# Optimization experiments

Hardware: AMD Instinct MI355X
Metric: run time of the kernel (lower is better)

The kernel has to match this reference:

```python
import jax, jax.numpy as jnp
import numpy as np

B, S, D_IN, D_OUT = 4, 4096, 768, 768

def setup_inputs() -> dict:
    key = jax.random.key(0)
    k1, k2, k3, k4 = jax.random.split(key, 4)
    x = jax.random.normal(k1, (B, S, D_IN), dtype=jnp.float32)
    # Stored as [d_in, d_out]; torch Linear computes x @ W.T with W [d_out, d_in],
    # which is equivalent to x @ W_here for a fresh random init.
    Wq = jax.random.normal(k2, (D_IN, D_OUT), dtype=jnp.float32) * (1.0 / np.sqrt(D_IN))
    Wk = jax.random.normal(k3, (D_IN, D_OUT), dtype=jnp.float32) * (1.0 / np.sqrt(D_IN))
    Wv = jax.random.normal(k4, (D_IN, D_OUT), dtype=jnp.float32) * (1.0 / np.sqrt(D_IN))
    return {"x": x, "Wq": Wq, "Wk": Wk, "Wv": Wv}

def reference(x, Wq, Wk, Wv):
    # x: [B, S, d_in]
    q = jnp.einsum('bsi,io->bso', x, Wq)  # [B, S, d_out]
    k = jnp.einsum('bsi,io->bso', x, Wk)
    v = jnp.einsum('bsi,io->bso', x, Wv)
    scale = 1.0 / jnp.sqrt(jnp.asarray(q.shape[-1], dtype=q.dtype))
    scores = jnp.einsum('bqd,bkd->bqk', q, k)  # [B, S, S]
    S_len = scores.shape[-1]
    causal = jnp.tril(jnp.ones((S_len, S_len), dtype=bool))  # True = keep
    scores = jnp.where(causal[None, :, :], scores, -jnp.inf)
    weights = jax.nn.softmax(scores * scale, axis=-1)
    # dropout p=0.0 -> identity
    return jnp.einsum('bqk,bkd->bqd', weights, v)
```

## Files before the change

### kernel.cpp

```cpp
#include <hip/hip_runtime.h>

typedef __attribute__((ext_vector_type(8))) short short8;
typedef __attribute__((ext_vector_type(4))) float f32x4;
typedef unsigned short u16;

#define MFMA_BF16 __builtin_amdgcn_mfma_f32_16x16x32_bf16

__device__ __forceinline__ u16 f2bf(float f) {
    unsigned int u = __builtin_bit_cast(unsigned int, f);
    u = (u + 0x7FFFu + ((u >> 16) & 1u)) >> 16;
    return (u16)u;
}

__device__ __forceinline__ void gl_lds16(const void* g, void* l) {
    __builtin_amdgcn_global_load_lds(
        (const __attribute__((address_space(1))) unsigned int*)g,
        (__attribute__((address_space(3))) unsigned int*)l, 16, 0, 0);
}

constexpr int D = 768;
constexpr int S = 4096;
constexpr float SCALE = 0.03608439182435161f;

__device__ __forceinline__ void tri_decode(int t, int& i, int& j) {
    i = (int)((sqrtf(8.0f * t + 1.0f) - 1.0f) * 0.5f);
    while ((i + 1) * (i + 2) / 2 <= t) ++i;
    while (i * (i + 1) / 2 > t) --i;
    j = t - i * (i + 1) / 2;
}

__global__ __launch_bounds__(256)
void conv_x(const float* __restrict__ x, u16* __restrict__ xb) {
    const size_t i = ((size_t)blockIdx.x * 256 + threadIdx.x) * 4;
    const float4 v = *reinterpret_cast<const float4*>(x + i);
    ushort4 o;
    o.x = f2bf(v.x); o.y = f2bf(v.y); o.z = f2bf(v.z); o.w = f2bf(v.w);
    *reinterpret_cast<ushort4*>(xb + i) = o;
}

__global__ __launch_bounds__(256)
void conv_wt(const float* __restrict__ Wq, const float* __restrict__ Wk,
             const float* __restrict__ Wv, u16* __restrict__ WT) {
    __shared__ float t[64][65];
    const int tid = threadIdx.x;
    const int k0 = blockIdx.x * 64, n0 = blockIdx.y * 64, z = blockIdx.z;
    const float* __restrict__ W = (z == 0) ? Wq : ((z == 1) ? Wk : Wv);
    #pragma unroll
    for (int i = 0; i < 4; ++i) {
        const int e = (i * 256 + tid) * 4;
        const int r = e >> 6, c = e & 63;
        const float4 v = *reinterpret_cast<const float4*>(W + (size_t)(k0 + r) * D + n0 + c);
        t[r][c] = v.x; t[r][c + 1] = v.y; t[r][c + 2] = v.z; t[r][c + 3] = v.w;
    }
    __syncthreads();
    u16* O = WT + (size_t)z * D * D;
    #pragma unroll
    for (int i = 0; i < 4; ++i) {
        const int e = (i * 256 + tid) * 4;
        const int n = e >> 6, kq = e & 63;
        ushort4 o;
        o.x = f2bf(t[kq + 0][n]); o.y = f2bf(t[kq + 1][n]);
        o.z = f2bf(t[kq + 2][n]); o.w = f2bf(t[kq + 3][n]);
        *reinterpret_cast<ushort4*>(O + (size_t)(n0 + n) * D + k0 + kq) = o;
    }
}

__global__ __launch_bounds__(256)
void qkv_gemm(const u16* __restrict__ xb, const u16* __restrict__ WT,
              u16* __restrict__ qo, u16* __restrict__ ko, u16* __restrict__ vt)
{
    __shared__ u16 sA[2][128 * 32];
    __shared__ u16 sB[2][128 * 32];
    const int tid  = threadIdx.x;
    const int lane = tid & 63;
    const int w    = tid >> 6;
    const int wr   = w >> 1, wc = w & 1;
    const int bm   = blockIdx.x * 128;
    const int bn   = blockIdx.y * 128;
    const int z    = blockIdx.z;
    const u16* __restrict__ A = xb;
    const u16* __restrict__ B = WT + (size_t)z * D * D;

    f32x4 acc[4][4] = {};

    auto stage = [&](int buf, int kc) {
        #pragma unroll
        for (int c = 0; c < 2; ++c) {
            const int e   = (c * 256 + tid) * 8;
            const int row = e >> 5, col = e & 31;
            gl_lds16(A + (size_t)(bm + row) * D + kc * 32 + col, &sA[buf][e]);
            gl_lds16(B + (size_t)(bn + row) * D + kc * 32 + col, &sB[buf][e]);
        }
    };

    stage(0, 0);
    __syncthreads();
    int cur = 0;
    for (int kc = 0; kc < 24; ++kc) {
        if (kc < 23) stage(cur ^ 1, kc + 1);
        short8 af[4], bf4[4];
        #pragma unroll
        for (int fr = 0; fr < 4; ++fr)
            af[fr] = *reinterpret_cast<const short8*>(&sA[cur][(wr * 64 + fr * 16 + (lane & 15)) * 32 + (lane >> 4) * 8]);
        #pragma unroll
        for (int fc = 0; fc < 4; ++fc)
            bf4[fc] = *reinterpret_cast<const short8*>(&sB[cur][(wc * 64 + fc * 16 + (lane & 15)) * 32 + (lane >> 4) * 8]);
        #pragma unroll
        for (int fr = 0; fr < 4; ++fr)
            #pragma unroll
            for (int fc = 0; fc < 4; ++fc)
                acc[fr][fc] = MFMA_BF16(af[fr], bf4[fc], acc[fr][fc], 0, 0, 0);
        __syncthreads();
        cur ^= 1;
    }

    #pragma unroll
    for (int fr = 0; fr < 4; ++fr) {
        #pragma unroll
        for (int fc = 0; fc < 4; ++fc) {
            #pragma unroll
            for (int r = 0; r < 4; ++r) {
                const int m = bm + wr * 64 + fr * 16 + (lane >> 4) * 4 + r;
                const int n = bn + wc * 64 + fc * 16 + (lane & 15);
                const u16 hv = f2bf(acc[fr][fc][r]);
                if (z == 0)      qo[(size_t)m * D + n] = hv;
                else if (z == 1) ko[(size_t)m * D + n] = hv;
                else {
                    const int bb = m >> 12;
                    const int s  = m & (S - 1);
                    vt[((size_t)bb * D + n) * S + s] = hv;
                }
            }
        }
    }
}

__global__ __launch_bounds__(256)
void qkt_gemm(const u16* __restrict__ Qg, const u16* __restrict__ Kg,
              u16* __restrict__ Pp, float* __restrict__ Lp)
{
    __shared__ u16 sA[2][128 * 32];
    __shared__ u16 sB[2][128 * 32];
    const int tid  = threadIdx.x;
    const int lane = tid & 63;
    const int w    = tid >> 6;
    const int wr   = w >> 1, wc = w & 1;
    int ti, tj;
    tri_decode(blockIdx.x, ti, tj);
    const int b = blockIdx.y;
    const u16* __restrict__ A = Qg + ((size_t)b * S + ti * 128) * D;
    const u16* __restrict__ B = Kg + ((size_t)b * S + tj * 128) * D;

    f32x4 acc[4][4] = {};

    auto stage = [&](int buf, int kc) {
        #pragma unroll
        for (int c = 0; c < 2; ++c) {
            const int e   = (c * 256 + tid) * 8;
            const int row = e >> 5, col = e & 31;
            gl_lds16(A + (size_t)row * D + kc * 32 + col, &sA[buf][e]);
            gl_lds16(B + (size_t)row * D + kc * 32 + col, &sB[buf][e]);
        }
    };

    stage(0, 0);
    __syncthreads();
    int cur = 0;
    for (int kc = 0; kc < 24; ++kc) {
        if (kc < 23) stage(cur ^ 1, kc + 1);
        short8 af[4], bf4[4];
        #pragma unroll
        for (int fr = 0; fr < 4; ++fr)
            af[fr] = *reinterpret_cast<const short8*>(&sA[cur][(wr * 64 + fr * 16 + (lane & 15)) * 32 + (lane >> 4) * 8]);
        #pragma unroll
        for (int fc = 0; fc < 4; ++fc)
            bf4[fc] = *reinterpret_cast<const short8*>(&sB[cur][(wc * 64 + fc * 16 + (lane & 15)) * 32 + (lane >> 4) * 8]);
        #pragma unroll
        for (int fr = 0; fr < 4; ++fr)
            #pragma unroll
            for (int fc = 0; fc < 4; ++fc)
                acc[fr][fc] = MFMA_BF16(af[fr], bf4[fc], acc[fr][fc], 0, 0, 0);
        __syncthreads();
        cur ^= 1;
    }

    const bool diag = (ti == tj);
    u16* outT = Pp + ((size_t)b * 528 + blockIdx.x) * 16384;
    #pragma unroll
    for (int fr = 0; fr < 4; ++fr) {
        #pragma unroll
        for (int r = 0; r < 4; ++r) {
            const int m = wr * 64 + fr * 16 + (lane >> 4) * 4 + r;
            float rs = 0.0f;
            #pragma unroll
            for (int fc = 0; fc < 4; ++fc) {
                const int n = wc * 64 + fc * 16 + (lane & 15);
                float p = __expf(acc[fr][fc][r] * SCALE - 10.0f);
                if (diag && n > m) p = 0.0f;
                rs += p;
                outT[m * 128 + n] = f2bf(p);
            }
            rs += __shfl_xor(rs, 1);
            rs += __shfl_xor(rs, 2);
            rs += __shfl_xor(rs, 4);
            rs += __shfl_xor(rs, 8);
            if ((lane & 15) == 0)
                Lp[(((size_t)b * 32 + tj) * 2 + wc) * 4096 + ti * 128 + m] = rs;
        }
    }
}

__global__ __launch_bounds__(256)
void reduce_l(const float* __restrict__ Lp, float* __restrict__ Li)
{
    const int row = blockIdx.x * 256 + threadIdx.x;
    const int b = row >> 12, r = row & 4095, imax = r >> 7;
    float l = 0.0f;
    for (int j = 0; j <= imax; ++j) {
        l += Lp[(((size_t)b * 32 + j) * 2 + 0) * 4096 + r];
        l += Lp[(((size_t)b * 32 + j) * 2 + 1) * 4096 + r];
    }
    Li[row] = 1.0f / l;
}

__global__ __launch_bounds__(512)
void pv_gemm(const u16* __restrict__ Pp, const u16* __restrict__ Vt,
             const float* __restrict__ Li, float* __restrict__ out)
{
    __shared__ u16 sV[2][192 * 64];
    __shared__ u16 sP[2][128 * 64];
    const int tid  = threadIdx.x;
    const int lane = tid & 63;
    const int w    = tid >> 6;
    const int wq   = w >> 2;
    const int wd   = w & 3;
    const int bid  = blockIdx.x;
    const int i    = 31 - (bid >> 4);
    const int b    = (bid >> 2) & 3;
    const int dq   = bid & 3;
    const int q0   = i * 128, d0 = dq * 192;
    const int nkt  = 2 * i + 2;
    const u16* __restrict__ Pt  = Pp + ((size_t)b * 528 + (size_t)i * (i + 1) / 2) * 16384;
    const u16* __restrict__ vtb = Vt + ((size_t)b * D + d0) * S;

    f32x4 acc[4][3] = {};

    auto stage_v = [&](int buf, int kt) {
        #pragma unroll
        for (int n = 0; n < 3; ++n) {
            const int ch  = n * 512 + tid;
            const int row = ch >> 3;
            const int csw = (ch & 7) ^ (row & 7);
            gl_lds16(vtb + (size_t)row * S + kt * 64 + csw * 8, &sV[buf][ch * 8]);
        }
    };
    auto stage_p = [&](int buf, int kt) {
        const u16* base = Pt + (size_t)(kt >> 1) * 16384 + (kt & 1) * 64;
        #pragma unroll
        for (int n = 0; n < 2; ++n) {
            const int ch  = n * 512 + tid;
            const int row = ch >> 3;
            const int csw = (ch & 7) ^ (row & 7);
            gl_lds16(base + row * 128 + csw * 8, &sP[buf][ch * 8]);
        }
    };

    stage_v(0, 0); stage_p(0, 0);
    __syncthreads();
    int cur = 0;
    for (int kt = 0; kt < nkt; ++kt) {
        if (kt + 1 < nkt) { stage_v(cur ^ 1, kt + 1); stage_p(cur ^ 1, kt + 1); }
        #pragma unroll
        for (int ks = 0; ks < 2; ++ks) {
            short8 a[4];
            #pragma unroll
            for (int fr = 0; fr < 4; ++fr) {
                const int row = wq * 64 + fr * 16 + (lane & 15);
                const int cch = (ks * 4 + (lane >> 4)) ^ (row & 7);
                a[fr] = *reinterpret_cast<const short8*>(&sP[cur][row * 64 + cch * 8]);
            }
            #pragma unroll
            for (int fc = 0; fc < 3; ++fc) {
                const int dr  = wd * 48 + fc * 16 + (lane & 15);
                const int vch = (ks * 4 + (lane >> 4)) ^ (dr & 7);
                const short8 bv = *reinterpret_cast<const short8*>(&sV[cur][dr * 64 + vch * 8]);
                #pragma unroll
                for (int fr = 0; fr < 4; ++fr)
                    acc[fr][fc] = MFMA_BF16(a[fr], bv, acc[fr][fc], 0, 0, 0);
            }
        }
        __syncthreads();
        cur ^= 1;
    }

    #pragma unroll
    for (int fr = 0; fr < 4; ++fr)
        #pragma unroll
        for (int rr = 0; rr < 4; ++rr) {
            const int row = q0 + wq * 64 + fr * 16 + (lane >> 4) * 4 + rr;
            const float linv = Li[b * 4096 + row];
            #pragma unroll
            for (int fc = 0; fc < 3; ++fc) {
                const int col = d0 + wd * 48 + fc * 16 + (lane & 15);
                out[((size_t)b * S + row) * D + col] = acc[fr][fc][rr] * linv;
            }
        }
}

extern "C" void kernel_launch(void* const* d_in, const int* in_sizes, int n_in,
                              void* d_out, int out_size, void* d_ws, size_t ws_size,
                              hipStream_t stream) {
    const float* x  = (const float*)d_in[0];
    const float* Wq = (const float*)d_in[1];
    const float* Wk = (const float*)d_in[2];
    const float* Wv = (const float*)d_in[3];
    float* out = (float*)d_out;

    const size_t SD = (size_t)16384 * 768;
    u16* q  = (u16*)d_ws;
    u16* k  = q  + SD;
    u16* vt = k  + SD;
    u16* xb = vt + SD;
    u16* WT = xb + SD;
    u16* Pp = WT + (size_t)3 * 768 * 768;
    float* Lp = (float*)(Pp + (size_t)4 * 528 * 16384);
    float* Li = Lp + (size_t)4 * 32 * 2 * 4096;
    (void)in_sizes; (void)n_in; (void)out_size; (void)ws_size;

    conv_x  <<<12288, 256, 0, stream>>>(x, xb);
    conv_wt <<<dim3(12, 12, 3), 256, 0, stream>>>(Wq, Wk, Wv, WT);
    qkv_gemm<<<dim3(128, 6, 3), 256, 0, stream>>>(xb, WT, q, k, vt);
    qkt_gemm<<<dim3(528, 4), 256, 0, stream>>>(q, k, Pp, Lp);
    reduce_l<<<64, 256, 0, stream>>>(Lp, Li);
    pv_gemm <<<512, 512, 0, stream>>>(Pp, vt, Li, out);
}
```

Baseline: 308.5 us.

## Enlarge QKV and QK^T GEMM tiles with swizzled LDS and deeper pipelining

The QKV projection and the causal QK^T score kernels move to 512-thread blocks with larger tiles (256x192 and 256x256) and K-chunks of 64. Shared memory uses an XOR-swizzled layout, the global-to-LDS loads are explicitly pipelined with vmcnt waits, raw barriers and setprio around the MFMA groups. The V transpose is no longer done by scattered stores in the GEMM epilogue. It becomes a separate LDS-based transpose kernel that uses the P buffer as scratch. The aim is more data reuse per load and less overhead from barriers and uncoalesced stores. The cost is an extra launch, more registers per thread, and extra work on the diagonal tiles that straddle the causal mask.

```diff
diff --git a/kernel.cpp b/kernel.cpp
--- a/kernel.cpp
+++ b/kernel.cpp
@@ -5,6 +5,9 @@
 typedef unsigned short u16;
 
 #define MFMA_BF16 __builtin_amdgcn_mfma_f32_16x16x32_bf16
+#define S_BARRIER()  asm volatile("s_barrier" ::: "memory")
+#define WAIT_LGKM0() asm volatile("s_waitcnt lgkmcnt(0)" ::: "memory")
+#define WAIT_VM(n)   asm volatile("s_waitcnt vmcnt(" #n ")" ::: "memory")
 
 __device__ __forceinline__ u16 f2bf(float f) {
     unsigned int u = __builtin_bit_cast(unsigned int, f);
@@ -27,6 +30,21 @@
     while ((i + 1) * (i + 2) / 2 <= t) ++i;
     while (i * (i + 1) / 2 > t) --i;
     j = t - i * (i + 1) / 2;
+}
+
+template<int NCH>
+__device__ __forceinline__ void stage64(const u16* __restrict__ g, u16* lds, int kcol, int tid) {
+    #pragma unroll
+    for (int i = 0; i < NCH; ++i) {
+        const int ch = i * 512 + tid;
+        const int row = ch >> 3, c = ch & 7;
+        const int cs = c ^ (row & 7);
+        gl_lds16(g + (size_t)row * 768 + kcol + cs * 8, lds + ch * 8);
+    }
+}
+__device__ __forceinline__ short8 ldsfrag(const u16* p, int row, int ks, int lane) {
+    const int cs = (ks * 4 + (lane >> 4)) ^ (row & 7);
+    return *reinterpret_cast<const short8*>(p + row * 64 + cs * 8);
 }
 
 __global__ __launch_bounds__(256)
@@ -65,161 +83,189 @@
     }
 }
 
+__global__ __launch_bounds__(512)
+void qkv_gemm(const u16* __restrict__ xb, const u16* __restrict__ WT,
+              u16* __restrict__ qo, u16* __restrict__ ko, u16* __restrict__ vb)
+{
+    __shared__ u16 sAb[2 * 256 * 64];
+    __shared__ u16 sBb[2 * 192 * 64];
+    const int tid = threadIdx.x, lane = tid & 63, w = tid >> 6;
+    const int wr = w >> 2, wn = w & 3;
+    const int bm = blockIdx.x * 256;
+    const u16* __restrict__ A = xb + (size_t)bm * 768;
+    const u16* __restrict__ B = WT + (size_t)blockIdx.y * 192 * 768;
+
+    f32x4 acc[8][3] = {};
+
+    stage64<4>(A, sAb, 0, tid);  stage64<3>(B, sBb, 0, tid);
+    stage64<4>(A, sAb + 16384, 64, tid);  stage64<3>(B, sBb + 12288, 64, tid);
+    WAIT_VM(7); S_BARRIER();
+
+    #pragma unroll 2
+    for (int kt = 0; kt < 12; ++kt) {
+        const int cur = kt & 1;
+        const u16* pA = sAb + cur * 16384;
+        const u16* pB = sBb + cur * 12288;
+        short8 a0[8], b0[3], a1[8], b1[3];
+        #pragma unroll
+        for (int fr = 0; fr < 8; ++fr) a0[fr] = ldsfrag(pA, wr * 128 + fr * 16 + (lane & 15), 0, lane);
+        #pragma unroll
+        for (int fc = 0; fc < 3; ++fc) b0[fc] = ldsfrag(pB, wn * 48 + fc * 16 + (lane & 15), 0, lane);
+        #pragma unroll
+        for (int fr = 0; fr < 8; ++fr)
+            #pragma unroll
+            for (int fc = 0; fc < 3; ++fc)
+                acc[fr][fc] = MFMA_BF16(a0[fr], b0[fc], acc[fr][fc], 0, 0, 0);
+        #pragma unroll
+        for (int fr = 0; fr < 8; ++fr) a1[fr] = ldsfrag(pA, wr * 128 + fr * 16 + (lane & 15), 1, lane);
+        #pragma unroll
+        for (int fc = 0; fc < 3; ++fc) b1[fc] = ldsfrag(pB, wn * 48 + fc * 16 + (lane & 15), 1, lane);
+        WAIT_LGKM0(); S_BARRIER();
+        if (kt < 10) { stage64<4>(A, sAb + cur * 16384, (kt + 2) * 64, tid);
+                       stage64<3>(B, sBb + cur * 12288, (kt + 2) * 64, tid); }
+        __builtin_amdgcn_s_setprio(1);
+        #pragma unroll
+        for (int fr = 0; fr < 8; ++fr)
+            #pragma unroll
+            for (int fc = 0; fc < 3; ++fc)
+                acc[fr][fc] = MFMA_BF16(a1[fr], b1[fc], acc[fr][fc], 0, 0, 0);
+        __builtin_amdgcn_s_setprio(0);
+        if (kt < 10) { WAIT_VM(7); } else { WAIT_VM(0); }
+        S_BARRIER();
+    }
+
+    const int z = blockIdx.y >> 2, nb = (blockIdx.y & 3) * 192;
+    u16* __restrict__ dst = (z == 0) ? qo : ((z == 1) ? ko : vb);
+    #pragma unroll
+    for (int fr = 0; fr < 8; ++fr)
+        #pragma unroll
+        for (int fc = 0; fc < 3; ++fc)
+            #pragma unroll
+            for (int r = 0; r < 4; ++r) {
+                const int m = bm + wr * 128 + fr * 16 + (lane >> 4) * 4 + r;
+                const int n = nb + wn * 48 + fc * 16 + (lane & 15);
+                dst[(size_t)m * 768 + n] = f2bf(acc[fr][fc][r]);
+            }
+}
+
 __global__ __launch_bounds__(256)
-void qkv_gemm(const u16* __restrict__ xb, const u16* __restrict__ WT,
-              u16* __restrict__ qo, u16* __restrict__ ko, u16* __restrict__ vt)
-{
-    __shared__ u16 sA[2][128 * 32];
-    __shared__ u16 sB[2][128 * 32];
-    const int tid  = threadIdx.x;
-    const int lane = tid & 63;
-    const int w    = tid >> 6;
-    const int wr   = w >> 1, wc = w & 1;
-    const int bm   = blockIdx.x * 128;
-    const int bn   = blockIdx.y * 128;
-    const int z    = blockIdx.z;
-    const u16* __restrict__ A = xb;
-    const u16* __restrict__ B = WT + (size_t)z * D * D;
-
-    f32x4 acc[4][4] = {};
-
-    auto stage = [&](int buf, int kc) {
-        #pragma unroll
-        for (int c = 0; c < 2; ++c) {
-            const int e   = (c * 256 + tid) * 8;
-            const int row = e >> 5, col = e & 31;
-            gl_lds16(A + (size_t)(bm + row) * D + kc * 32 + col, &sA[buf][e]);
-            gl_lds16(B + (size_t)(bn + row) * D + kc * 32 + col, &sB[buf][e]);
-        }
-    };
-
-    stage(0, 0);
+void tr_v(const u16* __restrict__ vb, u16* __restrict__ vt)
+{
+    __shared__ u16 t[64 * 64];
+    const int tid = threadIdx.x;
+    const int s0 = blockIdx.x * 64, d0 = blockIdx.y * 64, b = blockIdx.z;
+    const u16* __restrict__ src = vb + ((size_t)b * 4096 + s0) * 768 + d0;
+    #pragma unroll
+    for (int i = 0; i < 2; ++i) {
+        const int ch = i * 256 + tid, r = ch >> 3, c = ch & 7;
+        const int pc = c ^ ((r >> 3) & 7);
+        *reinterpret_cast<short8*>(&t[r * 64 + pc * 8]) =
+            *reinterpret_cast<const short8*>(src + (size_t)r * 768 + c * 8);
+    }
     __syncthreads();
-    int cur = 0;
-    for (int kc = 0; kc < 24; ++kc) {
-        if (kc < 23) stage(cur ^ 1, kc + 1);
-        short8 af[4], bf4[4];
-        #pragma unroll
-        for (int fr = 0; fr < 4; ++fr)
-            af[fr] = *reinterpret_cast<const short8*>(&sA[cur][(wr * 64 + fr * 16 + (lane & 15)) * 32 + (lane >> 4) * 8]);
-        #pragma unroll
-        for (int fc = 0; fc < 4; ++fc)
-            bf4[fc] = *reinterpret_cast<const short8*>(&sB[cur][(wc * 64 + fc * 16 + (lane & 15)) * 32 + (lane >> 4) * 8]);
-        #pragma unroll
-        for (int fr = 0; fr < 4; ++fr)
-            #pragma unroll
-            for (int fc = 0; fc < 4; ++fc)
-                acc[fr][fc] = MFMA_BF16(af[fr], bf4[fc], acc[fr][fc], 0, 0, 0);
-        __syncthreads();
-        cur ^= 1;
-    }
-
-    #pragma unroll
-    for (int fr = 0; fr < 4; ++fr) {
-        #pragma unroll
-        for (int fc = 0; fc < 4; ++fc) {
-            #pragma unroll
-            for (int r = 0; r < 4; ++r) {
-                const int m = bm + wr * 64 + fr * 16 + (lane >> 4) * 4 + r;
-                const int n = bn + wc * 64 + fc * 16 + (lane & 15);
-                const u16 hv = f2bf(acc[fr][fc][r]);
-                if (z == 0)      qo[(size_t)m * D + n] = hv;
-                else if (z == 1) ko[(size_t)m * D + n] = hv;
-                else {
-                    const int bb = m >> 12;
-                    const int s  = m & (S - 1);
-                    vt[((size_t)bb * D + n) * S + s] = hv;
-                }
-            }
-        }
-    }
-}
-
-__global__ __launch_bounds__(256)
+    u16* __restrict__ dstp = vt + ((size_t)b * 768 + d0) * 4096 + s0;
+    #pragma unroll
+    for (int i = 0; i < 2; ++i) {
+        const int ch = i * 256 + tid, dd = ch >> 3, sc = ch & 7;
+        short8 o;
+        #pragma unroll
+        for (int e = 0; e < 8; ++e)
+            o[e] = (short)t[(sc * 8 + e) * 64 + (((dd >> 3) ^ sc) & 7) * 8 + (dd & 7)];
+        *reinterpret_cast<short8*>(dstp + (size_t)dd * 4096 + sc * 8) = o;
+    }
+}
+
+__global__ __launch_bounds__(512)
 void qkt_gemm(const u16* __restrict__ Qg, const u16* __restrict__ Kg,
               u16* __restrict__ Pp, float* __restrict__ Lp)
 {
-    __shared__ u16 sA[2][128 * 32];
-    __shared__ u16 sB[2][128 * 32];
-    const int tid  = threadIdx.x;
-    const int lane = tid & 63;
-    const int w    = tid >> 6;
-    const int wr   = w >> 1, wc = w & 1;
+    __shared__ u16 sAb[2 * 256 * 64];
+    __shared__ u16 sBb[2 * 256 * 64];
+    const int tid = threadIdx.x, lane = tid & 63, w = tid >> 6;
+    const int wr = w >> 2, wn = w & 3;
     int ti, tj;
     tri_decode(blockIdx.x, ti, tj);
     const int b = blockIdx.y;
-    const u16* __restrict__ A = Qg + ((size_t)b * S + ti * 128) * D;
-    const u16* __restrict__ B = Kg + ((size_t)b * S + tj * 128) * D;
-
-    f32x4 acc[4][4] = {};
-
-    auto stage = [&](int buf, int kc) {
-        #pragma unroll
-        for (int c = 0; c < 2; ++c) {
-            const int e   = (c * 256 + tid) * 8;
-            const int row = e >> 5, col = e & 31;
-            gl_lds16(A + (size_t)row * D + kc * 32 + col, &sA[buf][e]);
-            gl_lds16(B + (size_t)row * D + kc * 32 + col, &sB[buf][e]);
-        }
-    };
-
-    stage(0, 0);
-    __syncthreads();
-    int cur = 0;
-    for (int kc = 0; kc < 24; ++kc) {
-        if (kc < 23) stage(cur ^ 1, kc + 1);
-        short8 af[4], bf4[4];
-        #pragma unroll
-        for (int fr = 0; fr < 4; ++fr)
-            af[fr] = *reinterpret_cast<const short8*>(&sA[cur][(wr * 64 + fr * 16 + (lane & 15)) * 32 + (lane >> 4) * 8]);
-        #pragma unroll
-        for (int fc = 0; fc < 4; ++fc)
-            bf4[fc] = *reinterpret_cast<const short8*>(&sB[cur][(wc * 64 + fc * 16 + (lane & 15)) * 32 + (lane >> 4) * 8]);
-        #pragma unroll
-        for (int fr = 0; fr < 4; ++fr)
+    const u16* __restrict__ A = Qg + ((size_t)b * S + ti * 256) * 768;
+    const u16* __restrict__ B = Kg + ((size_t)b * S + tj * 256) * 768;
+
+    f32x4 acc[8][4] = {};
+
+    stage64<4>(A, sAb, 0, tid);  stage64<4>(B, sBb, 0, tid);
+    stage64<4>(A, sAb + 16384, 64, tid);  stage64<4>(B, sBb + 16384, 64, tid);
+    WAIT_VM(8); S_BARRIER();
+
+    #pragma unroll 2
+    for (int kt = 0; kt < 12; ++kt) {
+        const int cur = kt & 1;
+        const u16* pA = sAb + cur * 16384;
+        const u16* pB = sBb + cur * 16384;
+        short8 a0[8], b0[4], a1[8], b1[4];
+        #pragma unroll
+        for (int fr = 0; fr < 8; ++fr) a0[fr] = ldsfrag(pA, wr * 128 + fr * 16 + (lane & 15), 0, lane);
+        #pragma unroll
+        for (int fc = 0; fc < 4; ++fc) b0[fc] = ldsfrag(pB, wn * 64 + fc * 16 + (lane & 15), 0, lane);
+        #pragma unroll
+        for (int fr = 0; fr < 8; ++fr)
             #pragma unroll
             for (int fc = 0; fc < 4; ++fc)
-                acc[fr][fc] = MFMA_BF16(af[fr], bf4[fc], acc[fr][fc], 0, 0, 0);
-        __syncthreads();
-        cur ^= 1;
+                acc[fr][fc] = MFMA_BF16(a0[fr], b0[fc], acc[fr][fc], 0, 0, 0);
+        #pragma unroll
+        for (int fr = 0; fr < 8; ++fr) a1[fr] = ldsfrag(pA, wr * 128 + fr * 16 + (lane & 15), 1, lane);
+        #pragma unroll
+        for (int fc = 0; fc < 4; ++fc) b1[fc] = ldsfrag(pB, wn * 64 + fc * 16 + (lane & 15), 1, lane);
+        WAIT_LGKM0(); S_BARRIER();
+        if (kt < 10) { stage64<4>(A, sAb + cur * 16384, (kt + 2) * 64, tid);
+                       stage64<4>(B, sBb + cur * 16384, (kt + 2) * 64, tid); }
+        __builtin_amdgcn_s_setprio(1);
+        #pragma unroll
+        for (int fr = 0; fr < 8; ++fr)
+            #pragma unroll
+            for (int fc = 0; fc < 4; ++fc)
+                acc[fr][fc] = MFMA_BF16(a1[fr], b1[fc], acc[fr][fc], 0, 0, 0);
+        __builtin_amdgcn_s_setprio(0);
+        if (kt < 10) { WAIT_VM(8); } else { WAIT_VM(0); }
+        S_BARRIER();
     }
 
     const bool diag = (ti == tj);
-    u16* outT = Pp + ((size_t)b * 528 + blockIdx.x) * 16384;
-    #pragma unroll
-    for (int fr = 0; fr < 4; ++fr) {
+    const int i128 = ti * 2 + wr;
+    const int j128 = tj * 2 + (wn >> 1);
+    const bool dostore = (j128 <= i128);
+    u16* __restrict__ tbase = Pp + ((size_t)b * 528 + (size_t)i128 * (i128 + 1) / 2 + j128) * 16384;
+    #pragma unroll
+    for (int fr = 0; fr < 8; ++fr)
         #pragma unroll
         for (int r = 0; r < 4; ++r) {
-            const int m = wr * 64 + fr * 16 + (lane >> 4) * 4 + r;
+            const int ml = wr * 128 + fr * 16 + (lane >> 4) * 4 + r;
+            const int gm = ti * 256 + ml;
             float rs = 0.0f;
             #pragma unroll
             for (int fc = 0; fc < 4; ++fc) {
-                const int n = wc * 64 + fc * 16 + (lane & 15);
+                const int nl = wn * 64 + fc * 16 + (lane & 15);
+                const int gn = tj * 256 + nl;
                 float p = __expf(acc[fr][fc][r] * SCALE - 10.0f);
-                if (diag && n > m) p = 0.0f;
+                if (diag && gn > gm) p = 0.0f;
                 rs += p;
-                outT[m * 128 + n] = f2bf(p);
+                if (dostore) tbase[(ml & 127) * 128 + (nl & 127)] = f2bf(p);
             }
             rs += __shfl_xor(rs, 1);
             rs += __shfl_xor(rs, 2);
             rs += __shfl_xor(rs, 4);
             rs += __shfl_xor(rs, 8);
             if ((lane & 15) == 0)
-                Lp[(((size_t)b * 32 + tj) * 2 + wc) * 4096 + ti * 128 + m] = rs;
-        }
-    }
+                Lp[((size_t)b * 64 + tj * 4 + wn) * 4096 + gm] = rs;
+        }
 }
 
 __global__ __launch_bounds__(256)
 void reduce_l(const float* __restrict__ Lp, float* __restrict__ Li)
 {
     const int row = blockIdx.x * 256 + threadIdx.x;
-    const int b = row >> 12, r = row & 4095, imax = r >> 7;
+    const int b = row >> 12, r = row & 4095, jm = r >> 6;
     float l = 0.0f;
-    for (int j = 0; j <= imax; ++j) {
-        l += Lp[(((size_t)b * 32 + j) * 2 + 0) * 4096 + r];
-        l += Lp[(((size_t)b * 32 + j) * 2 + 1) * 4096 + r];
-    }
+    for (int j = 0; j <= jm; ++j)
+        l += Lp[((size_t)b * 64 + j) * 4096 + r];
     Li[row] = 1.0f / l;
 }
 
@@ -323,14 +369,16 @@
     u16* xb = vt + SD;
     u16* WT = xb + SD;
     u16* Pp = WT + (size_t)3 * 768 * 768;
+    u16* vb = Pp;
     float* Lp = (float*)(Pp + (size_t)4 * 528 * 16384);
-    float* Li = Lp + (size_t)4 * 32 * 2 * 4096;
+    float* Li = Lp + (size_t)4 * 64 * 4096;
     (void)in_sizes; (void)n_in; (void)out_size; (void)ws_size;
 
     conv_x  <<<12288, 256, 0, stream>>>(x, xb);
     conv_wt <<<dim3(12, 12, 3), 256, 0, stream>>>(Wq, Wk, Wv, WT);
-    qkv_gemm<<<dim3(128, 6, 3), 256, 0, stream>>>(xb, WT, q, k, vt);
-    qkt_gemm<<<dim3(528, 4), 256, 0, stream>>>(q, k, Pp, Lp);
+    qkv_gemm<<<dim3(64, 12), 512, 0, stream>>>(xb, WT, q, k, vb);
+    tr_v    <<<dim3(64, 12, 4), 256, 0, stream>>>(vb, vt);
+    qkt_gemm<<<dim3(136, 4), 512, 0, stream>>>(q, k, Pp, Lp);
     reduce_l<<<64, 256, 0, stream>>>(Lp, Li);
     pv_gemm <<<512, 512, 0, stream>>>(Pp, vt, Li, out);
 }
```

New measurement: 376.1 us. 21.9% more time.
